# Optimization experiments

Measured on AMD Instinct MI355X. Metric: run time of the kernel, lower is better.

The kernel has to match this reference:

```python
import jax, jax.numpy as jnp
import numpy as np

# DCNv3 hyperparameters (from init_kwargs)
K = 3           # kernel_size
STRIDE = 1
PAD = 1
DIL = 1
GROUP = 4
GC = 16         # internelchannels = group_channels
CH = GROUP * GC # 64 internal channels
P = K * K       # sampling points per group
OFFSET_SCALE = 1.0


def setup_inputs() -> dict:
    key = jax.random.key(0)
    ks = jax.random.split(key, 8)
    B, H, W = 4, 128, 128
    cop_ch, aop_ch, out_ch = 64, 64, 64
    return {
        "x1": jax.random.normal(ks[0], (B, cop_ch, H, W), jnp.float32),
        "x2": jax.random.normal(ks[1], (B, aop_ch, H, W), jnp.float32),
        # value input projection (COP stream)
        "w_value": jax.random.normal(ks[2], (cop_ch, CH), jnp.float32) / np.sqrt(cop_ch),
        "b_value": jnp.zeros((CH,), jnp.float32),
        # offset/mask feature conv (AOP stream)
        "w_conv": jax.random.normal(ks[3], (K, K, aop_ch, CH), jnp.float32) / np.sqrt(K * K * aop_ch),
        "b_conv": jnp.zeros((CH,), jnp.float32),
        # offset head (small init so sampling stays near the regular grid)
        "w_offset": jax.random.normal(ks[4], (CH, GROUP * P * 2), jnp.float32) * 0.01,
        "b_offset": jnp.zeros((GROUP * P * 2,), jnp.float32),
        # mask head (softmax-normalized modulation)
        "w_mask": jax.random.normal(ks[5], (CH, GROUP * P), jnp.float32) * 0.1,
        "b_mask": jnp.zeros((GROUP * P,), jnp.float32),
        # output projection
        "w_out": jax.random.normal(ks[6], (CH, out_ch), jnp.float32) / np.sqrt(CH),
        "b_out": jnp.zeros((out_ch,), jnp.float32),
    }


def _bilinear_sample(vflat, x, y, Hp, Wp):
    """vflat: [B, Hp*Wp, G, gc]; x, y: [B, N, G] pixel coords in padded image.
    Returns [B, N, G, gc] zero-padded bilinear samples (grid_sample align_corners=False)."""
    x0 = jnp.floor(x)
    y0 = jnp.floor(y)
    out = jnp.zeros(vflat.shape[:1] + x.shape[1:] + vflat.shape[-1:], vflat.dtype)
    for dy in (0, 1):
        for dx in (0, 1):
            xi = x0 + dx
            yi = y0 + dy
            wgt = (1.0 - jnp.abs(x - xi)) * (1.0 - jnp.abs(y - yi))
            valid = (xi >= 0) & (xi < Wp) & (yi >= 0) & (yi < Hp)
            idx = (jnp.clip(yi, 0, Hp - 1) * Wp + jnp.clip(xi, 0, Wp - 1)).astype(jnp.int32)
            v = jnp.take_along_axis(vflat, idx[..., None], axis=1)  # [B,N,G,gc]
            out = out + v * (wgt * valid.astype(wgt.dtype))[..., None]
    return out


def reference(x1, x2, w_value, b_value, w_conv, b_conv,
              w_offset, b_offset, w_mask, b_mask, w_out, b_out):
    # NCHW -> NHWC (as in the torch wrapper)
    cop = jnp.transpose(x1, (0, 2, 3, 1))
    aop = jnp.transpose(x2, (0, 2, 3, 1))
    B, H, W, _ = cop.shape
    Hout = (H + 2 * PAD - DIL * (K - 1) - 1) // STRIDE + 1
    Wout = (W + 2 * PAD - DIL * (K - 1) - 1) // STRIDE + 1

    # value projection from COP stream: [B,H,W,CH]
    value = cop @ w_value + b_value

    # offset/mask branch from AOP stream
    feat = jax.lax.conv_general_dilated(
        aop, w_conv, (STRIDE, STRIDE), [(PAD, PAD), (PAD, PAD)],
        dimension_numbers=("NHWC", "HWIO", "NHWC")) + b_conv
    feat = jax.nn.gelu(feat)                                  # [B,Hout,Wout,CH]
    offset = (feat @ w_offset + b_offset).reshape(B, Hout, Wout, GROUP, P, 2)
    mask = jax.nn.softmax(
        (feat @ w_mask + b_mask).reshape(B, Hout, Wout, GROUP, P), axis=-1)

    # zero-pad the value map (DCNv3 pads input then samples in padded coords)
    vp = jnp.pad(value, ((0, 0), (PAD, PAD), (PAD, PAD), (0, 0)))
    Hp, Wp = H + 2 * PAD, W + 2 * PAD
    vflat = vp.reshape(B, Hp * Wp, GROUP, GC)

    # reference points + dilation grid (pixel coords in padded image)
    ref_x = (DIL * (K - 1) / 2 + jnp.arange(Wout, dtype=jnp.float32) * STRIDE)
    ref_y = (DIL * (K - 1) / 2 + jnp.arange(Hout, dtype=jnp.float32) * STRIDE)
    ky, kx = jnp.meshgrid(jnp.arange(K) - (K - 1) // 2,
                          jnp.arange(K) - (K - 1) // 2, indexing="ij")
    grid = jnp.stack([kx, ky], -1).reshape(P, 2).astype(jnp.float32) * DIL  # (dx,dy)

    x = (ref_x[None, None, :, None, None] + grid[None, None, None, None, :, 0]
         + offset[..., 0] * OFFSET_SCALE)                     # [B,Hout,Wout,G,P]
    y = (ref_y[None, :, None, None, None] + grid[None, None, None, None, :, 1]
         + offset[..., 1] * OFFSET_SCALE)

    # flatten to [B, N, G] with N = Hout*Wout*P (group axis kept last for gather)
    xr = jnp.transpose(x, (0, 1, 2, 4, 3)).reshape(B, Hout * Wout * P, GROUP)
    yr = jnp.transpose(y, (0, 1, 2, 4, 3)).reshape(B, Hout * Wout * P, GROUP)

    sampled = _bilinear_sample(vflat, xr, yr, Hp, Wp)         # [B,N,G,gc]
    sampled = sampled.reshape(B, Hout, Wout, P, GROUP, GC)

    out = jnp.einsum("bhwpgc,bhwgp->bhwgc", sampled, mask).reshape(B, Hout, Wout, CH)
    out = out @ w_out + b_out                                 # [B,Hout,Wout,out_ch]
    return jnp.transpose(out, (0, 3, 1, 2))                   # NHWC -> NCHW
```

## Files before the change

### kernel.cpp

```cpp
#include <hip/hip_runtime.h>
#include <cstdint>
#include <cstddef>

typedef float f4 __attribute__((ext_vector_type(4)));
typedef float f2 __attribute__((ext_vector_type(2)));
typedef float f32x4 __attribute__((ext_vector_type(4)));
typedef short short8 __attribute__((ext_vector_type(8)));
typedef unsigned int u32;
typedef unsigned short u16;
typedef u32 u32x4 __attribute__((ext_vector_type(4)));


__device__ __forceinline__ u16 f2bf(float f) {
    u32 u = __builtin_bit_cast(u32, f);
    return (u16)((u + 0x7FFFu + ((u >> 16) & 1u)) >> 16);
}

__device__ __forceinline__ int xcd_swz10(int d) {
    return ((d & 7) << 7) | (d >> 3);
}
__device__ __forceinline__ int xcd_swz12(int d) {
    return ((d & 7) << 9) | (d >> 3);
}

__global__ __launch_bounds__(256) void prep_all_k(float* __restrict__ vpad,
                                                  char* __restrict__ x2tp,
                                                  const float* __restrict__ wc,
                                                  const float* __restrict__ wo,
                                                  const float* __restrict__ wm,
                                                  char* __restrict__ wbfT,
                                                  char* __restrict__ whead) {
    int blk = blockIdx.x;
    if (blk < 260) {
        int i = blk * 256 + threadIdx.x;
        if (i >= 66560) return;
        int c4 = i & 15;
        int rest = i >> 4;
        int b = rest / 1040;
        int e = rest - b * 1040;
        int y, x;
        if (e < 132)      { y = 0;   x = e; }
        else if (e < 264) { y = 1;   x = e - 132; }
        else if (e < 396) { y = 130; x = e - 264; }
        else if (e < 528) { y = 131; x = e - 396; }
        else { int e2 = e - 528; y = 2 + (e2 >> 2); int m = e2 & 3;
               x = (m < 2) ? m : m + 128; }
        f4 z = {0.f, 0.f, 0.f, 0.f};
        *(f4*)(vpad + (((size_t)b * 17424 + (size_t)y * 132 + x) * 64 + c4 * 4)) = z;
    } else if (blk < 325) {
        int i = (blk - 260) * 256 + threadIdx.x;
        if (i >= 16512) return;
        int c8 = i & 7;
        int rest = i >> 3;
        int b = rest / 516;
        int e = rest - b * 516;
        int y, x;
        if (e < 130)      { y = 0;       x = e; }
        else if (e < 260) { y = 129;     x = e - 130; }
        else if (e < 388) { y = e - 259; x = 0; }
        else              { y = e - 387; x = 129; }
        u32x4 z = {0u, 0u, 0u, 0u};
        *(u32x4*)(x2tp + ((size_t)b * 16900 + (size_t)y * 130 + x) * 128 + c8 * 16) = z;
    } else if (blk < 397) {
        int i = (blk - 325) * 256 + threadIdx.x;
        int c = i / 288, kp = i - c * 288;
        int k = kp << 1;
        float f0 = wc[(size_t)k * 64 + c];
        float f1 = wc[(size_t)(k + 1) * 64 + c];
        u32 pk = (u32)f2bf(f0) | ((u32)f2bf(f1) << 16);
        *(u32*)(wbfT + (size_t)c * 1152 + kp * 4) = pk;
    } else {
        int i = (blk - 397) * 256 + threadIdx.x;
        int k = i & 63, col = i >> 6;
        float v = 0.f;
        if (col < 72)       v = wo[(size_t)k * 72 + col];
        else if (col < 108) v = wm[(size_t)k * 36 + col - 72];
        *(u16*)(whead + (size_t)(col * 64 + k) * 2) = f2bf(v);
    }
}

__global__ __launch_bounds__(256) void x2prep_k(const float* __restrict__ x2,
                                                char* __restrict__ x2tp) {
    __shared__ u32 tr[4096];
    int t = threadIdx.x;
    int y = blockIdx.x & 127, b = blockIdx.x >> 7;
    const float* xb = x2 + (size_t)b * 64 * 16384 + (size_t)y * 128;
    #pragma unroll 4
    for (int j = 0; j < 16; j++) {
        int idx = t + (j << 8);
        int x = idx & 127, cip = idx >> 7;
        int ci = cip << 1;
        float f0 = xb[(size_t)ci * 16384 + x];
        float f1 = xb[(size_t)(ci + 1) * 16384 + x];
        u32 pk = (u32)f2bf(f0) | ((u32)f2bf(f1) << 16);
        int key = (x + 1) & 7;
        int byt = x * 128 + (((ci >> 3) ^ key) << 4) + (ci & 7) * 2;
        tr[byt >> 2] = pk;
    }
    __syncthreads();
    const u32x4* src = (const u32x4*)tr;
    u32x4* dst = (u32x4*)(x2tp + ((size_t)(b * 130 + y + 1) * 130 + 1) * 128);
    #pragma unroll
    for (int j = 0; j < 4; j++) {
        int c = t + (j << 8);
        dst[c] = src[c];
    }
}

__global__ __launch_bounds__(256) void value_proj_k(const float* __restrict__ x1,
                                                    const float* __restrict__ wv,
                                                    const float* __restrict__ bv,
                                                    float* __restrict__ vpad) {
    __shared__ float xs[64][64];
    __shared__ float wsh[64][64];
    int tid = threadIdx.x;
    int bidx = xcd_swz10(blockIdx.x);
    int xb = bidx & 1;
    int y  = (bidx >> 1) & 127;
    int b  = bidx >> 8;
    int x0 = xb * 64;

    #pragma unroll
    for (int j = 0; j < 4; j++) {
        int chunk = tid + j * 256;
        int ci = chunk >> 4, p4 = chunk & 15;
        *(f4*)&xs[ci][p4 * 4] =
            *(const f4*)(x1 + (((size_t)b * 64 + ci) * 128 + y) * 128 + x0 + p4 * 4);
        *(f4*)&wsh[ci][p4 * 4] = *(const f4*)(wv + ci * 64 + p4 * 4);
    }
    __syncthreads();

    int c0 = (tid & 15) * 4, p0 = (tid >> 4) * 4;
    f4 bb = *(const f4*)(bv + c0);
    f4 acc[4];
    #pragma unroll
    for (int i = 0; i < 4; i++) acc[i] = bb;

    #pragma unroll
    for (int ci = 0; ci < 64; ci++) {
        f4 w4 = *(f4*)&wsh[ci][c0];
        f4 x4 = *(f4*)&xs[ci][p0];
        #pragma unroll
        for (int i = 0; i < 4; i++) acc[i] += x4[i] * w4;
    }

    #pragma unroll
    for (int i = 0; i < 4; i++) {
        int xp = x0 + p0 + i + 2;
        *(f4*)(vpad + (((size_t)b * 132 + (y + 2)) * 132 + xp) * 64 + c0) = acc[i];
    }
}

__global__ __launch_bounds__(256, 4) void conv_mfma_k(const char* __restrict__ x2tp,
                                                      const char* __restrict__ wbfT,
                                                      const float* __restrict__ bc,
                                                      char* __restrict__ featb) {
    __shared__ char slab[3 * 8448];
    int tid = threadIdx.x;
    int l = tid & 63, w = tid >> 6;
    int bidx = xcd_swz10(blockIdx.x);
    int xb = bidx & 1, y = (bidx >> 1) & 127, b = bidx >> 8;
    int x0 = xb << 6;

    const char* gr = x2tp + ((size_t)(b * 130 + y) * 130 + x0) * 128;
    for (int q = w; q < 27; q += 4) {
        int r = q / 9, cq = q - r * 9;
        int nb = (cq < 8) ? 1024 : 256;
        if (l * 16 < nb) {
            const char* g = gr + (size_t)r * (130 * 128) + cq * 1024 + l * 16;
            char* p = slab + r * 8448 + cq * 1024 + l * 16;
            __builtin_amdgcn_global_load_lds(
                (const __attribute__((address_space(1))) u32*)g,
                (__attribute__((address_space(3))) u32*)p, 16, 0, 0);
        }
    }
    __syncthreads();

    int m0 = w << 4;
    int r16 = l & 15, g16 = l >> 4;
    f32x4 acc[4] = {{0.f,0.f,0.f,0.f},{0.f,0.f,0.f,0.f},
                    {0.f,0.f,0.f,0.f},{0.f,0.f,0.f,0.f}};
    const char* wb = wbfT + (size_t)r16 * 1152 + g16 * 16;

    #pragma unroll
    for (int s = 0; s < 18; s++) {
        const int t9 = s >> 1;
        const int ky = t9 / 3, kx = t9 - ky * 3;
        const int ci0g = (s & 1) * 4;
        int x_sl = m0 + r16 + kx;
        int go = (ci0g + g16) ^ (x_sl & 7);
        short8 a = *(const short8*)(slab + ky * 8448 + x_sl * 128 + go * 16);
        #pragma unroll
        for (int cb = 0; cb < 4; cb++) {
            short8 bf = *(const short8*)(wb + (size_t)cb * (16 * 1152) + s * 64);
            acc[cb] = __builtin_amdgcn_mfma_f32_16x16x32_bf16(a, bf, acc[cb], 0, 0, 0);
        }
    }

    const float kA = 0.7978845608028654f, kB = 0.044715f;
    char* fp = featb + ((size_t)b * 16384 + (size_t)y * 128 + x0 + m0) * 128;
    #pragma unroll
    for (int cb = 0; cb < 4; cb++) {
        float bcv = bc[cb * 16 + r16];
        #pragma unroll
        for (int j = 0; j < 4; j++) {
            float v = acc[cb][j] + bcv;
            float z = kA * (v + kB * v * v * v);
            float e = __expf(2.f * z);
            float th = 1.f - 2.f / (e + 1.f);
            float o = 0.5f * v * (1.f + th);
            *(u16*)(fp + (size_t)(g16 * 4 + j) * 128 + (cb * 16 + r16) * 2) = f2bf(o);
        }
    }
}

__global__ __launch_bounds__(128, 7) void dcn_fused_v6(const char* __restrict__ featb,
                                                       const float* __restrict__ vpad,
                                                       const char* __restrict__ whead,
                                                       const float* __restrict__ bo,
                                                       const float* __restrict__ bm,
                                                       const float* __restrict__ wout,
                                                       const float* __restrict__ bout,
                                                       float* __restrict__ out) {
    __shared__ float off_s [2][8][74];
    __shared__ float msk_s [2][8][38];
    __shared__ float samp_s[2][8][64];

    int tid = threadIdx.x;
    int w = tid >> 6, l = tid & 63;
    int blk = xcd_swz12(blockIdx.x);
    int b = blk >> 10, y = (blk >> 3) & 127, xo = blk & 7;
    int x0w = xo * 16 + w * 8;
    int pix0 = ((b << 7) + y) * 128 + x0w;

    int r = l & 15, q = l >> 4;

    const char* fpt = featb + (size_t)(pix0 + r) * 128 + q * 16;
    short8 a0 = *(const short8*)fpt;
    short8 a1 = *(const short8*)(fpt + 64);

    const char* wh = whead + (size_t)r * 128 + q * 16;
    f32x4 hc[7];
    #pragma unroll
    for (int t = 0; t < 7; t++) {
        short8 b0 = *(const short8*)(wh + t * 2048);
        short8 b1 = *(const short8*)(wh + t * 2048 + 64);
        f32x4 z = {0.f, 0.f, 0.f, 0.f};
        z = __builtin_amdgcn_mfma_f32_16x16x32_bf16(a0, b0, z, 0, 0, 0);
        hc[t] = __builtin_amdgcn_mfma_f32_16x16x32_bf16(a1, b1, z, 0, 0, 0);
    }

    if (q < 2) {
        #pragma unroll
        for (int t = 0; t < 7; t++) {
            int col = t * 16 + r;
            float bias = 0.f;
            if (col < 72)        bias = bo[col];
            else if (col < 108)  bias = bm[col - 72];
            #pragma unroll
            for (int j = 0; j < 4; j++) {
                int px = q * 4 + j;
                float v = hc[t][j] + bias;
                if (col < 72)       off_s[w][px][col] = v;
                else if (col < 108) msk_s[w][px][col - 72] = v;
            }
        }
    }

    if (l < 32) {
        int px = l >> 2, g = l & 3;
        float m[9];
        #pragma unroll
        for (int p = 0; p < 9; p++) m[p] = msk_s[w][px][g * 9 + p];
        float mx = m[0];
        #pragma unroll
        for (int p = 1; p < 9; p++) mx = fmaxf(mx, m[p]);
        float s = 0.f;
        #pragma unroll
        for (int p = 0; p < 9; p++) { m[p] = __expf(m[p] - mx); s += m[p]; }
        float inv = 1.f / s;
        #pragma unroll
        for (int p = 0; p < 9; p++) msk_s[w][px][g * 9 + p] = m[p] * inv;
    }

    {
        int cc4 = l & 3, g = (l >> 2) & 3, pxs = l >> 4;
        const float* vb = vpad + (size_t)b * 17424 * 64 + g * 16 + cc4 * 4;
        #pragma unroll
        for (int j = 0; j < 2; j++) {
            int px = pxs * 2 + j;
            int xpix = x0w + px;
            f4 acc = {0.f, 0.f, 0.f, 0.f};
            #pragma unroll
            for (int p = 0; p < 9; p++) {
                const int kx = p % 3, ky = p / 3;
                f2 oxy = *(const f2*)&off_s[w][px][g * 18 + 2 * p];
                float mv = msk_s[w][px][g * 9 + p];
                float sx = (float)(xpix + kx) + oxy[0];
                float sy = (float)(y + ky) + oxy[1];
                float xf = floorf(sx), yf = floorf(sy);
                float fx = sx - xf, fy = sy - yf;
                int ix = (int)xf, iy = (int)yf;
                int e0 = (iy * 132 + ix + 133) << 6;
                const float* pa = vb + e0;
                f4 v00 = *(const f4*)pa;
                f4 v01 = *(const f4*)(pa + 64);
                f4 v10 = *(const f4*)(pa + 8448);
                f4 v11 = *(const f4*)(pa + 8512);
                float wy0 = mv * (1.f - fy), wy1 = mv * fy;
                float w00 = wy0 * (1.f - fx), w01 = wy0 * fx;
                float w10 = wy1 * (1.f - fx), w11 = wy1 * fx;
                #pragma unroll
                for (int c = 0; c < 4; c++)
                    acc[c] = fmaf(w00, v00[c],
                             fmaf(w01, v01[c],
                             fmaf(w10, v10[c],
                             fmaf(w11, v11[c], acc[c]))));
            }
            *(f4*)&samp_s[w][px][g * 16 + cc4 * 4] = acc;
        }
    }

    float oa[8];
    float bv = bout[l];
    #pragma unroll
    for (int px = 0; px < 8; px++) oa[px] = bv;
    const float* pw = wout + l;
    #pragma unroll 4
    for (int k4 = 0; k4 < 16; k4++) {
        float w0 = pw[0], w1 = pw[64], w2 = pw[128], w3 = pw[192];
        pw += 256;
        #pragma unroll
        for (int px = 0; px < 8; px++) {
            f4 sv = *(f4*)&samp_s[w][px][k4 * 4];
            oa[px] = fmaf(sv[0], w0, fmaf(sv[1], w1,
                     fmaf(sv[2], w2, fmaf(sv[3], w3, oa[px]))));
        }
    }

    float* op = out + ((size_t)b * 64 + l) * 16384 + y * 128 + x0w;
    f4 o0 = {oa[0], oa[1], oa[2], oa[3]};
    f4 o1 = {oa[4], oa[5], oa[6], oa[7]};
    *(f4*)op       = o0;
    *(f4*)(op + 4) = o1;
}

extern "C" void kernel_launch(void* const* d_in, const int* in_sizes, int n_in,
                              void* d_out, int out_size, void* d_ws, size_t ws_size,
                              hipStream_t stream) {
    const float* x1       = (const float*)d_in[0];
    const float* x2       = (const float*)d_in[1];
    const float* w_value  = (const float*)d_in[2];
    const float* b_value  = (const float*)d_in[3];
    const float* w_conv   = (const float*)d_in[4];
    const float* b_conv   = (const float*)d_in[5];
    const float* w_offset = (const float*)d_in[6];
    const float* b_offset = (const float*)d_in[7];
    const float* w_mask   = (const float*)d_in[8];
    const float* b_mask   = (const float*)d_in[9];
    const float* w_out    = (const float*)d_in[10];
    const float* b_out    = (const float*)d_in[11];

    float* vpad  = (float*)d_ws;
    char*  featb = (char*)d_ws + 17842176;
    char*  x2tp  = (char*)d_ws + 26230784;
    char*  wbfT  = (char*)d_ws + 34883584;
    char*  whead = (char*)d_ws + 34957312;
    float* outp  = (float*)d_out;

    hipLaunchKernelGGL(prep_all_k,   dim3(425),  dim3(256), 0, stream,
                       vpad, x2tp, w_conv, w_offset, w_mask, wbfT, whead);
    hipLaunchKernelGGL(x2prep_k,     dim3(512),  dim3(256), 0, stream, x2, x2tp);
    hipLaunchKernelGGL(value_proj_k, dim3(1024), dim3(256), 0, stream,
                       x1, w_value, b_value, vpad);
    hipLaunchKernelGGL(conv_mfma_k,  dim3(1024), dim3(256), 0, stream,
                       x2tp, wbfT, b_conv, featb);
    hipLaunchKernelGGL(dcn_fused_v6, dim3(4096), dim3(128), 0, stream,
                       featb, vpad, whead, b_offset, b_mask, w_out, b_out, outp);
}
```

Measured before the change: 202.2 us.

## Retile conv and DCN kernels, swap MFMA operands for packed feature stores

The conv kernel now uses 128-thread blocks that each cover 32 output pixels with a smaller LDS slab, and its load loop is flattened. It swaps the MFMA A/B operands so each lane holds consecutive channels, which allows packed 8-byte bf16 stores in place of scattered 2-byte stores. The fused DCN kernel goes back to 256-thread blocks covering 32 pixels per row segment, with larger shared buffers and a new XCD swizzle. The feature load now repeats 8 pixels across the 16 MFMA rows. The aim is fewer, wider global writes and a different occupancy/work-per-block balance. The risk is reduced LDS-load reuse in conv and altered occupancy in the DCN kernel.

```diff
diff --git a/kernel.cpp b/kernel.cpp
--- a/kernel.cpp
+++ b/kernel.cpp
@@ -8,6 +8,7 @@
 typedef short short8 __attribute__((ext_vector_type(8)));
 typedef unsigned int u32;
 typedef unsigned short u16;
+typedef u32 u32x2 __attribute__((ext_vector_type(2)));
 typedef u32 u32x4 __attribute__((ext_vector_type(4)));
 
 
@@ -19,8 +20,8 @@
 __device__ __forceinline__ int xcd_swz10(int d) {
     return ((d & 7) << 7) | (d >> 3);
 }
-__device__ __forceinline__ int xcd_swz12(int d) {
-    return ((d & 7) << 9) | (d >> 3);
+__device__ __forceinline__ int xcd_swz11(int d) {
+    return ((d & 7) << 8) | (d >> 3);
 }
 
 __global__ __launch_bounds__(256) void prep_all_k(float* __restrict__ vpad,
@@ -151,28 +152,25 @@
     }
 }
 
-__global__ __launch_bounds__(256, 4) void conv_mfma_k(const char* __restrict__ x2tp,
+__global__ __launch_bounds__(128, 4) void conv_mfma_k(const char* __restrict__ x2tp,
                                                       const char* __restrict__ wbfT,
                                                       const float* __restrict__ bc,
                                                       char* __restrict__ featb) {
-    __shared__ char slab[3 * 8448];
+    __shared__ char slab[3 * 4352];
     int tid = threadIdx.x;
     int l = tid & 63, w = tid >> 6;
-    int bidx = xcd_swz10(blockIdx.x);
-    int xb = bidx & 1, y = (bidx >> 1) & 127, b = bidx >> 8;
-    int x0 = xb << 6;
+    int bidx = xcd_swz11(blockIdx.x);
+    int xq = bidx & 3, y = (bidx >> 2) & 127, b = bidx >> 9;
+    int x0 = xq << 5;
 
     const char* gr = x2tp + ((size_t)(b * 130 + y) * 130 + x0) * 128;
-    for (int q = w; q < 27; q += 4) {
-        int r = q / 9, cq = q - r * 9;
-        int nb = (cq < 8) ? 1024 : 256;
-        if (l * 16 < nb) {
-            const char* g = gr + (size_t)r * (130 * 128) + cq * 1024 + l * 16;
-            char* p = slab + r * 8448 + cq * 1024 + l * 16;
-            __builtin_amdgcn_global_load_lds(
-                (const __attribute__((address_space(1))) u32*)g,
-                (__attribute__((address_space(3))) u32*)p, 16, 0, 0);
-        }
+    for (int q = tid; q < 816; q += 128) {
+        int r = q / 272, c = q - r * 272;
+        const char* g = gr + (size_t)r * (130 * 128) + c * 16;
+        char* p = slab + q * 16;
+        __builtin_amdgcn_global_load_lds(
+            (const __attribute__((address_space(1))) u32*)g,
+            (__attribute__((address_space(3))) u32*)p, 16, 0, 0);
     }
     __syncthreads();
 
@@ -189,32 +187,34 @@
         const int ci0g = (s & 1) * 4;
         int x_sl = m0 + r16 + kx;
         int go = (ci0g + g16) ^ (x_sl & 7);
-        short8 a = *(const short8*)(slab + ky * 8448 + x_sl * 128 + go * 16);
+        short8 a = *(const short8*)(slab + ky * 4352 + x_sl * 128 + go * 16);
         #pragma unroll
         for (int cb = 0; cb < 4; cb++) {
             short8 bf = *(const short8*)(wb + (size_t)cb * (16 * 1152) + s * 64);
-            acc[cb] = __builtin_amdgcn_mfma_f32_16x16x32_bf16(a, bf, acc[cb], 0, 0, 0);
+            acc[cb] = __builtin_amdgcn_mfma_f32_16x16x32_bf16(bf, a, acc[cb], 0, 0, 0);
         }
     }
 
     const float kA = 0.7978845608028654f, kB = 0.044715f;
-    char* fp = featb + ((size_t)b * 16384 + (size_t)y * 128 + x0 + m0) * 128;
+    char* fp = featb + ((size_t)b * 16384 + (size_t)y * 128 + x0 + m0 + r16) * 128;
     #pragma unroll
     for (int cb = 0; cb < 4; cb++) {
-        float bcv = bc[cb * 16 + r16];
+        f4 b4 = *(const f4*)(bc + cb * 16 + g16 * 4);
+        u16 h[4];
         #pragma unroll
         for (int j = 0; j < 4; j++) {
-            float v = acc[cb][j] + bcv;
+            float v = acc[cb][j] + b4[j];
             float z = kA * (v + kB * v * v * v);
             float e = __expf(2.f * z);
             float th = 1.f - 2.f / (e + 1.f);
-            float o = 0.5f * v * (1.f + th);
-            *(u16*)(fp + (size_t)(g16 * 4 + j) * 128 + (cb * 16 + r16) * 2) = f2bf(o);
-        }
-    }
-}
-
-__global__ __launch_bounds__(128, 7) void dcn_fused_v6(const char* __restrict__ featb,
+            h[j] = f2bf(0.5f * v * (1.f + th));
+        }
+        u32x2 pk = {(u32)h[0] | ((u32)h[1] << 16), (u32)h[2] | ((u32)h[3] << 16)};
+        *(u32x2*)(fp + cb * 32 + g16 * 8) = pk;
+    }
+}
+
+__global__ __launch_bounds__(256, 6) void dcn_fused_v5(const char* __restrict__ featb,
                                                        const float* __restrict__ vpad,
                                                        const char* __restrict__ whead,
                                                        const float* __restrict__ bo,
@@ -222,20 +222,20 @@
                                                        const float* __restrict__ wout,
                                                        const float* __restrict__ bout,
                                                        float* __restrict__ out) {
-    __shared__ float off_s [2][8][74];
-    __shared__ float msk_s [2][8][38];
-    __shared__ float samp_s[2][8][64];
+    __shared__ float off_s [4][8][74];
+    __shared__ float msk_s [4][8][38];
+    __shared__ float samp_s[4][8][64];
 
     int tid = threadIdx.x;
     int w = tid >> 6, l = tid & 63;
-    int blk = xcd_swz12(blockIdx.x);
-    int b = blk >> 10, y = (blk >> 3) & 127, xo = blk & 7;
-    int x0w = xo * 16 + w * 8;
+    int blk = xcd_swz11(blockIdx.x);
+    int b = blk >> 9, y = (blk >> 2) & 127, xq = blk & 3;
+    int x0w = xq * 32 + w * 8;
     int pix0 = ((b << 7) + y) * 128 + x0w;
 
     int r = l & 15, q = l >> 4;
 
-    const char* fpt = featb + (size_t)(pix0 + r) * 128 + q * 16;
+    const char* fpt = featb + (size_t)(pix0 + (r & 7)) * 128 + q * 16;
     short8 a0 = *(const short8*)fpt;
     short8 a1 = *(const short8*)(fpt + 64);
 
@@ -373,8 +373,8 @@
     hipLaunchKernelGGL(x2prep_k,     dim3(512),  dim3(256), 0, stream, x2, x2tp);
     hipLaunchKernelGGL(value_proj_k, dim3(1024), dim3(256), 0, stream,
                        x1, w_value, b_value, vpad);
-    hipLaunchKernelGGL(conv_mfma_k,  dim3(1024), dim3(256), 0, stream,
+    hipLaunchKernelGGL(conv_mfma_k,  dim3(2048), dim3(128), 0, stream,
                        x2tp, wbfT, b_conv, featb);
-    hipLaunchKernelGGL(dcn_fused_v6, dim3(4096), dim3(128), 0, stream,
+    hipLaunchKernelGGL(dcn_fused_v5, dim3(2048), dim3(256), 0, stream,
                        featb, vpad, whead, b_offset, b_mask, w_out, b_out, outp);
 }
```

Result: no change. 199.8 us (-1.2%).
